# Performance work log

Hardware: AMD Instinct MI355X
Metric: run time of the kernel (lower is better)

## Reference

```python
import jax, jax.numpy as jnp
import numpy as np

B, S, IN, HID, H, D, FF = 8, 2048, 512, 512, 8, 64, 2048
EPS = 1e-5


def layer_norm(x, g, b):
    m = jnp.mean(x, axis=-1, keepdims=True)
    v = jnp.mean(jnp.square(x - m), axis=-1, keepdims=True)
    return (x - m) * jax.lax.rsqrt(v + EPS) * g + b


def delta_rule(q, k, v, beta):
    # q,k,v: [S,B,H,D]; beta: [S,B,H,1]
    # W_t = W_{t-1} + beta_t*(v_t - W_{t-1} k_t) k_t^T ; out_t = W_t q_t
    def step(W, inp):
        qt, kt, vt, bt = inp
        wk = jnp.einsum('bhde,bhe->bhd', W, kt)
        v_new = bt * (vt - wk)
        W = W + jnp.einsum('bhd,bhe->bhde', v_new, kt)
        out = jnp.einsum('bhde,bhe->bhd', W, qt)
        return W, out

    bsz = q.shape[1]
    W0 = jnp.zeros((bsz, H, D, D), dtype=q.dtype)
    _, outs = jax.lax.scan(step, W0, (q, k, v, beta))
    return outs  # [S,B,H,D]


def fast_ff(x, ln_g, ln_b, slow_w, out_w):
    # x: [S,B,HID]
    slen, bsz, _ = x.shape
    h = layer_norm(x, ln_g, ln_b)
    qkvb = jnp.einsum('sbi,oi->sbo', h, slow_w).reshape(slen, bsz, H, 3 * D + 1)
    q, k, v, beta = jnp.split(qkvb, [D, 2 * D, 3 * D], axis=-1)
    q = jax.nn.softmax(q, axis=-1)
    k = jax.nn.softmax(k, axis=-1)
    beta = jax.nn.sigmoid(beta)
    attn = delta_rule(q, k, v, beta)  # [S,B,H,D]
    o = jnp.einsum('sbd,od->sbo', attn.reshape(slen, bsz, H * D), out_w)
    return x + o


def ffn(x, ln_g, ln_b, w1, b1, w2, b2):
    h = layer_norm(x, ln_g, ln_b)
    h = jax.nn.relu(jnp.einsum('sbi,fi->sbf', h, w1) + b1)
    return x + jnp.einsum('sbf,of->sbo', h, w2) + b2


def setup_inputs() -> dict:
    key = jax.random.key(0)
    ks = jax.random.split(key, 8)
    s = 0.02
    return {
        'x': jax.random.normal(ks[0], (B, S, IN), jnp.float32),
        'ip_w': s * jax.random.normal(ks[1], (HID, IN), jnp.float32),
        'ip_b': jnp.zeros((HID,), jnp.float32),
        'fw_ln_g': jnp.ones((2, HID), jnp.float32),
        'fw_ln_b': jnp.zeros((2, HID), jnp.float32),
        'fw_slow_w': s * jax.random.normal(ks[2], (2, H * (3 * D + 1), HID), jnp.float32),
        'fw_out_w': s * jax.random.normal(ks[3], (2, HID, H * D), jnp.float32),
        'ff_ln_g': jnp.ones((HID,), jnp.float32),
        'ff_ln_b': jnp.zeros((HID,), jnp.float32),
        'ff_w1': s * jax.random.normal(ks[4], (FF, HID), jnp.float32),
        'ff_b1': jnp.zeros((FF,), jnp.float32),
        'ff_w2': s * jax.random.normal(ks[5], (HID, FF), jnp.float32),
        'ff_b2': jnp.zeros((HID,), jnp.float32),
    }


def reference(x, ip_w, ip_b, fw_ln_g, fw_ln_b, fw_slow_w, fw_out_w,
              ff_ln_g, ff_ln_b, ff_w1, ff_b1, ff_w2, ff_b2):
    out = jnp.einsum('bsi,hi->bsh', x, ip_w) + ip_b  # input_proj
    out = out.transpose(1, 0, 2)  # [S,B,HID]
    out = fast_ff(out, fw_ln_g[0], fw_ln_b[0], fw_slow_w[0], fw_out_w[0])
    out = ffn(out, ff_ln_g, ff_ln_b, ff_w1, ff_b1, ff_w2, ff_b2)
    out = fast_ff(out, fw_ln_g[1], fw_ln_b[1], fw_slow_w[1], fw_out_w[1])
    return out.transpose(1, 0, 2)  # [B,S,HID]
```

## Files before the change

### kernel.cpp

```cpp
#include <hip/hip_runtime.h>
#include <hip/hip_bf16.h>

#define B_    8
#define S_    2048
#define HID_  512
#define H_    8
#define D_    64
#define FF_   2048
#define QN_   1664
#define NCH_  32
#define SLOWSTRIDE (1544 * 512)

typedef unsigned short u16;
typedef __attribute__((ext_vector_type(8))) short short8;
typedef __attribute__((ext_vector_type(4))) float f32x4;

__device__ __forceinline__ u16 f2bf(float x) {
  unsigned u = __builtin_bit_cast(unsigned, x);
  unsigned r = (u + 0x7FFFu + ((u >> 16) & 1u)) >> 16;
  return (u16)r;
}
__device__ __forceinline__ float bf2f(u16 v) {
  return __builtin_bit_cast(float, (unsigned)v << 16);
}
__device__ __forceinline__ void gload16(const void* g, void* l) {
  __builtin_amdgcn_global_load_lds(
      (const __attribute__((address_space(1))) unsigned int*)g,
      (__attribute__((address_space(3))) unsigned int*)l, 16, 0, 0);
}

template<int FS, int GS>
__device__ __forceinline__ void prod64(const u16* __restrict__ F,
                                       const u16* __restrict__ G,
                                       int wrow0, int lane, f32x4 acc[4])
{
  short8 f0 = *(const short8*)&F[(wrow0 + (lane & 15)) * FS + ((lane >> 4) * 8)];
  short8 f1 = *(const short8*)&F[(wrow0 + (lane & 15)) * FS + 32 + ((lane >> 4) * 8)];
  #pragma unroll
  for (int c0 = 0; c0 < 4; ++c0) {
    short8 g0 = *(const short8*)&G[(c0 * 16 + (lane & 15)) * GS + ((lane >> 4) * 8)];
    short8 g1 = *(const short8*)&G[(c0 * 16 + (lane & 15)) * GS + 32 + ((lane >> 4) * 8)];
    acc[c0] = __builtin_amdgcn_mfma_f32_16x16x32_bf16(f0, g0, acc[c0], 0, 0, 0);
    acc[c0] = __builtin_amdgcn_mfma_f32_16x16x32_bf16(f1, g1, acc[c0], 0, 0, 0);
  }
}

template<bool BIAS, bool RELU, bool RES, bool OUTBF, bool TRANS, bool QKVB>
__global__ __launch_bounds__(256, 4) void gemm_bf(
    const u16* __restrict__ A, const u16* __restrict__ W,
    const float* __restrict__ bias, const float* __restrict__ res,
    void* __restrict__ Cout, int M, int N, int K)
{
  __shared__ __align__(16) u16 SH[16384];
  const int tid = threadIdx.x, lane = tid & 63, wv = tid >> 6;
  const int bm = blockIdx.y * 128, bn = blockIdx.x * 128;
  const int wr = wv >> 1, wc = wv & 1;
  const int row16 = lane & 15, kg = lane >> 4;
  const int srow = lane >> 2;
  const int ssoff = ((lane & 3) ^ (srow & 3)) * 16;

  f32x4 acc[4][4] = {};
  const int ktiles = K >> 5;

  auto STAGE = [&](int buf, int kt) {
    u16* As = &SH[buf * 8192];
    u16* Bs = &SH[buf * 8192 + 4096];
    #pragma unroll
    for (int i = 0; i < 2; ++i) {
      const int r = i * 64 + wv * 16;
      const char* ga = (const char*)(A + (size_t)(bm + r + srow) * K + (size_t)kt * 32) + ssoff;
      gload16(ga, &As[r * 32]);
      const char* gw = (const char*)(W + (size_t)(bn + r + srow) * K + (size_t)kt * 32) + ssoff;
      gload16(gw, &Bs[r * 32]);
    }
  };

  STAGE(0, 0);
  __syncthreads();
  int buf = 0;
  for (int kt = 0; kt < ktiles; ++kt) {
    if (kt + 1 < ktiles) STAGE(buf ^ 1, kt + 1);
    const u16* As = &SH[buf * 8192];
    const u16* Bs = &SH[buf * 8192 + 4096];
    short8 af[4], bf_[4];
    #pragma unroll
    for (int m = 0; m < 4; ++m) {
      const int lrow = wr * 64 + m * 16 + row16;
      af[m] = *(const short8*)&As[lrow * 32 + (kg ^ (lrow & 3)) * 8];
    }
    #pragma unroll
    for (int n = 0; n < 4; ++n) {
      const int lrow = wc * 64 + n * 16 + row16;
      bf_[n] = *(const short8*)&Bs[lrow * 32 + (kg ^ (lrow & 3)) * 8];
    }
    #pragma unroll
    for (int m = 0; m < 4; ++m)
      #pragma unroll
      for (int n = 0; n < 4; ++n)
        acc[m][n] = __builtin_amdgcn_mfma_f32_16x16x32_bf16(af[m], bf_[n], acc[m][n], 0, 0, 0);
    __syncthreads();
    buf ^= 1;
  }

  if (QKVB) {
    const int span0 = bn + wc * 64;
    #pragma unroll
    for (int m = 0; m < 4; ++m) {
      #pragma unroll
      for (int j = 0; j < 4; ++j) {
        if (span0 < 1024) {
          float v0 = acc[m][0][j], v1 = acc[m][1][j];
          float v2 = acc[m][2][j], v3 = acc[m][3][j];
          float mx = fmaxf(fmaxf(v0, v1), fmaxf(v2, v3));
          #pragma unroll
          for (int off = 1; off < 16; off <<= 1) mx = fmaxf(mx, __shfl_xor(mx, off));
          float e0 = __expf(v0 - mx), e1 = __expf(v1 - mx);
          float e2 = __expf(v2 - mx), e3 = __expf(v3 - mx);
          float s = (e0 + e1) + (e2 + e3);
          #pragma unroll
          for (int off = 1; off < 16; off <<= 1) s += __shfl_xor(s, off);
          float r = 1.f / s;
          acc[m][0][j] = e0 * r; acc[m][1][j] = e1 * r;
          acc[m][2][j] = e2 * r; acc[m][3][j] = e3 * r;
        } else if (span0 >= 1536) {
          #pragma unroll
          for (int n = 0; n < 4; ++n)
            acc[m][n][j] = 1.f / (1.f + __expf(-acc[m][n][j]));
        }
      }
    }
  }

  float* LD = (float*)SH;
  #pragma unroll
  for (int p = 0; p < 4; ++p) {
    if (p) __syncthreads();
    if (wr == (p >> 1)) {
      #pragma unroll
      for (int mm = 0; mm < 2; ++mm) {
        const int m = (p & 1) * 2 + mm;
        #pragma unroll
        for (int n = 0; n < 4; ++n)
          #pragma unroll
          for (int j = 0; j < 4; ++j)
            LD[(mm * 16 + kg * 4 + j) * 132 + wc * 64 + n * 16 + row16] = acc[m][n][j];
      }
    }
    __syncthreads();
    #pragma unroll
    for (int step = 0; step < 4; ++step) {
      int linear = step * 256 + tid;
      int row = linear >> 5, q = linear & 31;
      float4 v = *(const float4*)&LD[row * 132 + q * 4];
      const int grow = bm + p * 32 + row;
      const int gcol = bn + q * 4;
      if (BIAS) {
        float4 b4 = *(const float4*)&bias[gcol];
        v.x += b4.x; v.y += b4.y; v.z += b4.z; v.w += b4.w;
      }
      if (RES) {
        float4 r4 = *(const float4*)&res[(size_t)grow * N + gcol];
        v.x += r4.x; v.y += r4.y; v.z += r4.z; v.w += r4.w;
      }
      if (RELU) {
        v.x = fmaxf(v.x, 0.f); v.y = fmaxf(v.y, 0.f);
        v.z = fmaxf(v.z, 0.f); v.w = fmaxf(v.w, 0.f);
      }
      size_t gr = TRANS ? ((size_t)(grow & 7) * S_ + (grow >> 3)) : (size_t)grow;
      if (OUTBF) {
        uint2 pk;
        pk.x = (unsigned)f2bf(v.x) | ((unsigned)f2bf(v.y) << 16);
        pk.y = (unsigned)f2bf(v.z) | ((unsigned)f2bf(v.w) << 16);
        *(uint2*)&((u16*)Cout)[gr * N + gcol] = pk;
      } else {
        *(float4*)&((float*)Cout)[gr * N + gcol] = v;
      }
    }
  }
}

__global__ __launch_bounds__(256) void conv_w(const float* __restrict__ s,
                                              u16* __restrict__ d, int n, int npad)
{
  int i = blockIdx.x * 256 + threadIdx.x;
  if (i < npad) d[i] = (i < n) ? f2bf(s[i]) : (u16)0;
}

__global__ __launch_bounds__(256) void conv_slow(const float* __restrict__ s,
                                                 u16* __restrict__ d)
{
  int r = blockIdx.x;
  int src;
  if (r < 512)       src = (r >> 6) * 193 + (r & 63);
  else if (r < 1024) src = ((r - 512) >> 6) * 193 + 64 + (r & 63);
  else if (r < 1536) src = ((r - 1024) >> 6) * 193 + 128 + (r & 63);
  else if (r < 1544) src = (r - 1536) * 193 + 192;
  else               src = -1;
  for (int c = threadIdx.x; c < 512; c += 256)
    d[(size_t)r * 512 + c] = (src >= 0) ? f2bf(s[(size_t)src * 512 + c]) : (u16)0;
}

__global__ __launch_bounds__(64) void conv_x(const float* __restrict__ x,
                                             u16* __restrict__ xbf)
{
  size_t m = blockIdx.x;
  size_t s = m >> 3, b = m & 7;
  const float4* src = (const float4*)(x + (b * (size_t)S_ + s) * HID_);
  float4 v0 = src[threadIdx.x], v1 = src[64 + threadIdx.x];
  u16* dst = xbf + m * HID_;
  uint2 p0, p1;
  p0.x = (unsigned)f2bf(v0.x) | ((unsigned)f2bf(v0.y) << 16);
  p0.y = (unsigned)f2bf(v0.z) | ((unsigned)f2bf(v0.w) << 16);
  p1.x = (unsigned)f2bf(v1.x) | ((unsigned)f2bf(v1.y) << 16);
  p1.y = (unsigned)f2bf(v1.z) | ((unsigned)f2bf(v1.w) << 16);
  *(uint2*)&dst[threadIdx.x * 4] = p0;
  *(uint2*)&dst[256 + threadIdx.x * 4] = p1;
}

__global__ __launch_bounds__(64) void ln_bf(const float* __restrict__ x,
    const float* __restrict__ g, const float* __restrict__ bt,
    u16* __restrict__ o)
{
  size_t row = blockIdx.x;
  int lane = threadIdx.x;
  const float4* xr = (const float4*)(x + row * HID_);
  float4 v0 = xr[lane];
  float4 v1 = xr[64 + lane];
  float s  = v0.x + v0.y + v0.z + v0.w + v1.x + v1.y + v1.z + v1.w;
  float ss = v0.x*v0.x + v0.y*v0.y + v0.z*v0.z + v0.w*v0.w
           + v1.x*v1.x + v1.y*v1.y + v1.z*v1.z + v1.w*v1.w;
  #pragma unroll
  for (int off = 32; off; off >>= 1) {
    s  += __shfl_xor(s, off);
    ss += __shfl_xor(ss, off);
  }
  float mean = s * (1.f / HID_);
  float inv  = rsqrtf(ss * (1.f / HID_) - mean * mean + 1e-5f);
  const float4* gv = (const float4*)g;
  const float4* bv = (const float4*)bt;
  float4 g0 = gv[lane], g1 = gv[64 + lane];
  float4 b0 = bv[lane], b1 = bv[64 + lane];
  uint2 p0, p1;
  p0.x = (unsigned)f2bf((v0.x - mean) * inv * g0.x + b0.x)
       | ((unsigned)f2bf((v0.y - mean) * inv * g0.y + b0.y) << 16);
  p0.y = (unsigned)f2bf((v0.z - mean) * inv * g0.z + b0.z)
       | ((unsigned)f2bf((v0.w - mean) * inv * g0.w + b0.w) << 16);
  p1.x = (unsigned)f2bf((v1.x - mean) * inv * g1.x + b1.x)
       | ((unsigned)f2bf((v1.y - mean) * inv * g1.y + b1.y) << 16);
  p1.y = (unsigned)f2bf((v1.z - mean) * inv * g1.z + b1.z)
       | ((unsigned)f2bf((v1.w - mean) * inv * g1.w + b1.w) << 16);
  u16* ov = o + row * HID_;
  *(uint2*)&ov[lane * 4] = p0;
  *(uint2*)&ov[256 + lane * 4] = p1;
}

__global__ __launch_bounds__(256, 3) void delta_p1(const u16* __restrict__ qf,
                                                   u16* __restrict__ MTg,
                                                   u16* __restrict__ Ng,
                                                   u16* __restrict__ CKg,
                                                   u16* __restrict__ U0Tg)
{
  __shared__ __align__(16) u16 Kb[64 * 72];
  __shared__ __align__(16) u16 AmKT[64 * 72];
  __shared__ __align__(16) u16 stV[16 * 72];
  __shared__ __align__(16) u16 stK[16 * 72];
  __shared__ __align__(16) u16 CKTb[64 * 72];
  __shared__ __align__(16) u16 U0Tb[64 * 72];
  __shared__ float bet[64];

  const int id5 = blockIdx.x, bh = id5 >> 5;
  const int b = bh & 7, h = bh >> 3, t0 = (id5 & 31) * 64;
  const int tid = threadIdx.x, lane = tid & 63, wv = tid >> 6;
  const int wid = wv, wrow0 = wv * 16;
  const size_t mb = (size_t)id5 * 4096;

  #pragma unroll
  for (int p = 0; p < 2; ++p) {
    int linear = p * 256 + tid, row = linear >> 3, seg = linear & 7;
    uint4 k4 = *(const uint4*)&qf[((size_t)(t0 + row) * B_ + b) * QN_ + 512 + h * 64 + seg * 8];
    *(short8*)&Kb[row * 72 + seg * 8] = __builtin_bit_cast(short8, k4);
  }
  if (tid < 64) bet[tid] = bf2f(qf[((size_t)(t0 + tid) * B_ + b) * QN_ + 1536 + h]);
  __syncthreads();

  {
    f32x4 a[4] = {};
    prod64<72, 72>(Kb, Kb, wrow0, lane, a);
    #pragma unroll
    for (int c0 = 0; c0 < 4; ++c0)
      #pragma unroll
      for (int j = 0; j < 4; ++j) {
        int row = wrow0 + (lane >> 4) * 4 + j, col = c0 * 16 + (lane & 15);
        AmKT[row * 72 + col] = f2bf(bet[row] * a[c0][j]);
      }
  }

  float uv[16], uk[16];
  #pragma unroll
  for (int i = 0; i < 16; ++i) {
    const int row = wrow0 + i;
    const float bt_ = bet[row];
    uv[i] = bt_ * bf2f(qf[((size_t)(t0 + row) * B_ + b) * QN_ + 1024 + h * 64 + lane]);
    uk[i] = bt_ * bf2f(Kb[row * 72 + lane]);
  }
  __syncthreads();

  #pragma unroll 1
  for (int blk = 0; blk < 4; ++blk) {
    if (wid == blk) {
      const int r0 = blk * 16;
      #pragma unroll
      for (int jj = 0; jj < 15; ++jj) {
        #pragma unroll
        for (int t = jj + 1; t < 16; ++t) {
          float a = bf2f(AmKT[(r0 + t) * 72 + r0 + jj]);
          uv[t] = fmaf(-a, uv[jj], uv[t]);
          uk[t] = fmaf(-a, uk[jj], uk[t]);
        }
      }
      #pragma unroll
      for (int i = 0; i < 16; ++i) {
        stV[i * 72 + lane] = f2bf(uv[i]);
        stK[i * 72 + lane] = f2bf(uk[i]);
      }
    }
    __syncthreads();
    if (wid > blk) {
      const int r0 = blk * 16;
      #pragma unroll
      for (int jj = 0; jj < 16; ++jj) {
        float sv = bf2f(stV[jj * 72 + lane]);
        float sk = bf2f(stK[jj * 72 + lane]);
        #pragma unroll
        for (int i = 0; i < 16; ++i) {
          float a = bf2f(AmKT[(wrow0 + i) * 72 + r0 + jj]);
          uv[i] = fmaf(-a, sv, uv[i]);
          uk[i] = fmaf(-a, sk, uk[i]);
        }
      }
    }
    __syncthreads();
  }

  #pragma unroll
  for (int i = 0; i < 16; ++i) {
    const int row = wrow0 + i;
    u16 ck = f2bf(uk[i]), u0 = f2bf(uv[i]);
    CKg[mb + (size_t)row * 64 + lane] = ck;
    CKTb[lane * 72 + row] = ck;
    U0Tb[lane * 72 + row] = u0;
  }
  {
    const int prow = tid >> 2, pc0 = (tid & 3) * 16;
    #pragma unroll
    for (int i = 0; i < 16; ++i)
      AmKT[prow * 72 + pc0 + i] = Kb[(pc0 + i) * 72 + prow];
  }
  __syncthreads();

  {
    f32x4 am[4] = {}, an[4] = {};
    prod64<72, 72>(AmKT, CKTb, wrow0, lane, am);
    prod64<72, 72>(U0Tb, AmKT, wrow0, lane, an);
    #pragma unroll
    for (int c0 = 0; c0 < 4; ++c0)
      #pragma unroll
      for (int j = 0; j < 4; ++j) {
        int row = wrow0 + (lane >> 4) * 4 + j, col = c0 * 16 + (lane & 15);
        MTg[mb + (size_t)row * 64 + col] = f2bf(am[c0][j]);
        Ng[mb + (size_t)row * 64 + col]  = f2bf(an[c0][j]);
      }
    const int prow = tid >> 2, pc0 = (tid & 3) * 16;
    short8 a0 = *(const short8*)&U0Tb[prow * 72 + pc0];
    short8 a1 = *(const short8*)&U0Tb[prow * 72 + pc0 + 8];
    *(uint4*)&U0Tg[mb + prow * 64 + pc0]     = __builtin_bit_cast(uint4, a0);
    *(uint4*)&U0Tg[mb + prow * 64 + pc0 + 8] = __builtin_bit_cast(uint4, a1);
  }
}

__global__ __launch_bounds__(256, 1) void delta_p2(const u16* __restrict__ MTg,
                                                   const u16* __restrict__ Ng,
                                                   u16* __restrict__ Wsnap)
{
  __shared__ float Ws[64][65];
  __shared__ __align__(16) u16 Wbf[64 * 72];
  __shared__ __align__(16) u16 MTb[64 * 72];
  __shared__ __align__(16) u16 Nb[64 * 72];
  const int bh = blockIdx.x;
  const int tid = threadIdx.x, lane = tid & 63, wv = tid >> 6, wrow0 = wv * 16;
  const int prow = tid >> 2, pc0 = (tid & 3) * 16;

  for (int i = tid; i < 64 * 65; i += 256) (&Ws[0][0])[i] = 0.f;
  for (int i = tid; i < 64 * 72; i += 256) Wbf[i] = 0;
  __syncthreads();

  size_t base = (size_t)bh * NCH_ * 4096;
  uint4 rm0 = *(const uint4*)&MTg[base + prow * 64 + pc0];
  uint4 rm1 = *(const uint4*)&MTg[base + prow * 64 + pc0 + 8];
  uint4 rn0 = *(const uint4*)&Ng[base + prow * 64 + pc0];
  uint4 rn1 = *(const uint4*)&Ng[base + prow * 64 + pc0 + 8];

  for (int j = 0; j < NCH_; ++j) {
    *(short8*)&MTb[prow * 72 + pc0]     = __builtin_bit_cast(short8, rm0);
    *(short8*)&MTb[prow * 72 + pc0 + 8] = __builtin_bit_cast(short8, rm1);
    *(short8*)&Nb[prow * 72 + pc0]      = __builtin_bit_cast(short8, rn0);
    *(short8*)&Nb[prow * 72 + pc0 + 8]  = __builtin_bit_cast(short8, rn1);
    {
      size_t sb = base + (size_t)j * 4096;
      short8 w0 = *(const short8*)&Wbf[prow * 72 + pc0];
      short8 w1 = *(const short8*)&Wbf[prow * 72 + pc0 + 8];
      *(uint4*)&Wsnap[sb + prow * 64 + pc0]     = __builtin_bit_cast(uint4, w0);
      *(uint4*)&Wsnap[sb + prow * 64 + pc0 + 8] = __builtin_bit_cast(uint4, w1);
    }
    if (j + 1 < NCH_) {
      size_t nb2 = base + (size_t)(j + 1) * 4096;
      rm0 = *(const uint4*)&MTg[nb2 + prow * 64 + pc0];
      rm1 = *(const uint4*)&MTg[nb2 + prow * 64 + pc0 + 8];
      rn0 = *(const uint4*)&Ng[nb2 + prow * 64 + pc0];
      rn1 = *(const uint4*)&Ng[nb2 + prow * 64 + pc0 + 8];
    }
    __syncthreads();
    f32x4 a[4] = {};
    prod64<72, 72>(Wbf, MTb, wrow0, lane, a);
    #pragma unroll
    for (int c0 = 0; c0 < 4; ++c0)
      #pragma unroll
      for (int jj = 0; jj < 4; ++jj) {
        int row = wrow0 + (lane >> 4) * 4 + jj, col = c0 * 16 + (lane & 15);
        float w = Ws[row][col] + bf2f(Nb[row * 72 + col]) - a[c0][jj];
        Ws[row][col] = w;
        Wbf[row * 72 + col] = f2bf(w);
      }
    __syncthreads();
  }
}

__global__ __launch_bounds__(256, 2) void delta_p3(const u16* __restrict__ qf,
                                                   const u16* __restrict__ Wsnap,
                                                   const u16* __restrict__ CKg,
                                                   const u16* __restrict__ U0Tg,
                                                   u16* __restrict__ attnb)
{
  __shared__ __align__(16) u16 Qb[64 * 72];
  __shared__ __align__(16) u16 Kb[64 * 72];
  __shared__ __align__(16) u16 W0b[64 * 72];
  __shared__ __align__(16) u16 CKb[64 * 72];
  __shared__ __align__(16) u16 U0Tb[64 * 72];
  __shared__ __align__(16) u16 Gb[64 * 72];
  __shared__ __align__(16) u16 UTb[64 * 72];

  const int id5 = blockIdx.x, bh = id5 >> 5;
  const int b = bh & 7, h = bh >> 3, t0 = (id5 & 31) * 64;
  const int tid = threadIdx.x, lane = tid & 63, wv = tid >> 6, wrow0 = wv * 16;
  const int prow = tid >> 2, pc0 = (tid & 3) * 16;
  const size_t mb = (size_t)id5 * 4096;

  #pragma unroll
  for (int p = 0; p < 2; ++p) {
    int linear = p * 256 + tid, row = linear >> 3, seg = linear & 7;
    size_t gb = ((size_t)(t0 + row) * B_ + b) * QN_;
    uint4 q4 = *(const uint4*)&qf[gb + h * 64 + seg * 8];
    uint4 k4 = *(const uint4*)&qf[gb + 512 + h * 64 + seg * 8];
    uint4 w4 = *(const uint4*)&Wsnap[mb + (size_t)row * 64 + seg * 8];
    *(short8*)&Qb[row * 72 + seg * 8]  = __builtin_bit_cast(short8, q4);
    *(short8*)&Kb[row * 72 + seg * 8]  = __builtin_bit_cast(short8, k4);
    *(short8*)&W0b[row * 72 + seg * 8] = __builtin_bit_cast(short8, w4);
  }
  {
    uint4 c0v = *(const uint4*)&CKg[mb + prow * 64 + pc0];
    uint4 c1v = *(const uint4*)&CKg[mb + prow * 64 + pc0 + 8];
    uint4 u0v = *(const uint4*)&U0Tg[mb + prow * 64 + pc0];
    uint4 u1v = *(const uint4*)&U0Tg[mb + prow * 64 + pc0 + 8];
    *(short8*)&CKb[prow * 72 + pc0]      = __builtin_bit_cast(short8, c0v);
    *(short8*)&CKb[prow * 72 + pc0 + 8]  = __builtin_bit_cast(short8, c1v);
    *(short8*)&U0Tb[prow * 72 + pc0]     = __builtin_bit_cast(short8, u0v);
    *(short8*)&U0Tb[prow * 72 + pc0 + 8] = __builtin_bit_cast(short8, u1v);
  }
  __syncthreads();

  f32x4 ag[4] = {}, ac[4] = {}, ab[4] = {};
  prod64<72, 72>(Qb, Kb, wrow0, lane, ag);
  prod64<72, 72>(W0b, CKb, wrow0, lane, ac);
  prod64<72, 72>(Qb, W0b, wrow0, lane, ab);

  #pragma unroll
  for (int c0 = 0; c0 < 4; ++c0)
    #pragma unroll
    for (int j = 0; j < 4; ++j) {
      int row = wrow0 + (lane >> 4) * 4 + j, col = c0 * 16 + (lane & 15);
      Gb[row * 72 + col]  = f2bf(col <= row ? ag[c0][j] : 0.f);
      UTb[row * 72 + col] = f2bf(bf2f(U0Tb[row * 72 + col]) - ac[c0][j]);
    }
  __syncthreads();

  prod64<72, 72>(Gb, UTb, wrow0, lane, ab);

  #pragma unroll
  for (int c0 = 0; c0 < 4; ++c0)
    #pragma unroll
    for (int j = 0; j < 4; ++j) {
      int row = wrow0 + (lane >> 4) * 4 + j, col = c0 * 16 + (lane & 15);
      attnb[((size_t)(t0 + row) * B_ + b) * HID_ + h * 64 + col] = f2bf(ab[c0][j]);
    }
}

extern "C" void kernel_launch(void* const* d_in, const int* in_sizes, int n_in,
                              void* d_out, int out_size, void* d_ws, size_t ws_size,
                              hipStream_t stream)
{
  const float* x        = (const float*)d_in[0];
  const float* ip_w     = (const float*)d_in[1];
  const float* ip_b     = (const float*)d_in[2];
  const float* fw_ln_g  = (const float*)d_in[3];
  const float* fw_ln_b  = (const float*)d_in[4];
  const float* fw_slow_w = (const float*)d_in[5];
  const float* fw_out_w  = (const float*)d_in[6];
  const float* ff_ln_g  = (const float*)d_in[7];
  const float* ff_ln_b  = (const float*)d_in[8];
  const float* ff_w1    = (const float*)d_in[9];
  const float* ff_b1    = (const float*)d_in[10];
  const float* ff_w2    = (const float*)d_in[11];
  const float* ff_b2    = (const float*)d_in[12];
  float* out = (float*)d_out;

  const int M = B_ * S_;
  const size_t matN = (size_t)64 * NCH_ * 4096;

  const size_t nIp = 512 * 512, nOut = 512 * 512;
  const size_t nSlow = (size_t)QN_ * 512;
  const size_t nW1 = (size_t)FF_ * 512, nW2 = (size_t)512 * FF_;
  const size_t nXbf = (size_t)M * HID_;
  const size_t poolElems = nIp + 2 * nSlow + 2 * nOut + nW1 + nW2 + nXbf + matN;

  size_t need = (size_t)M * HID_ * 4
              + ((size_t)M * QN_ + 2 * matN + poolElems) * 2;
  if (ws_size < need) return;

  float* cur   = (float*)d_ws;
  u16*   qkvbf = (u16*)(cur + (size_t)M * HID_);
  u16*   attnSlot = qkvbf + (size_t)M * QN_;
  u16*   MTg   = attnSlot;
  u16*   Ng    = MTg + matN;
  u16*   attnb = attnSlot;
  u16*   CKg   = (u16*)out;
  u16*   U0Tg  = CKg + matN;
  u16*   tmpbf = (u16*)out;
  u16*   hiddenb = qkvbf;

  u16* pool = attnSlot + 2 * matN;
  u16* ipwb   = pool;               pool += nIp;
  u16* slowb0 = pool;               pool += nSlow;
  u16* slowb1 = pool;               pool += nSlow;
  u16* outwb0 = pool;               pool += nOut;
  u16* outwb1 = pool;               pool += nOut;
  u16* w1b    = pool;               pool += nW1;
  u16* w2b    = pool;               pool += nW2;
  u16* Wsnap  = pool;               pool += matN;
  u16* xbf    = pool;

  dim3 blk(256);

  conv_w<<<(nIp + 255) / 256, blk, 0, stream>>>(ip_w, ipwb, nIp, nIp);
  conv_slow<<<QN_, blk, 0, stream>>>(fw_slow_w, slowb0);
  conv_slow<<<QN_, blk, 0, stream>>>(fw_slow_w + (size_t)SLOWSTRIDE, slowb1);
  conv_w<<<(nOut + 255) / 256, blk, 0, stream>>>(fw_out_w, outwb0, nOut, nOut);
  conv_w<<<(nOut + 255) / 256, blk, 0, stream>>>(fw_out_w + (size_t)512 * 512, outwb1, nOut, nOut);
  conv_w<<<(nW1 + 255) / 256, blk, 0, stream>>>(ff_w1, w1b, nW1, nW1);
  conv_w<<<(nW2 + 255) / 256, blk, 0, stream>>>(ff_w2, w2b, nW2, nW2);
  conv_x<<<M, 64, 0, stream>>>(x, xbf);

  gemm_bf<true, false, false, false, false, false><<<dim3(4, 128), blk, 0, stream>>>(
      xbf, ipwb, ip_b, nullptr, cur, M, HID_, HID_);

  for (int layer = 0; layer < 2; ++layer) {
    u16* slowb = layer ? slowb1 : slowb0;
    u16* outwb = layer ? outwb1 : outwb0;

    ln_bf<<<M, 64, 0, stream>>>(cur, fw_ln_g + layer * HID_, fw_ln_b + layer * HID_, tmpbf);
    gemm_bf<false, false, false, true, false, true><<<dim3(13, 128), blk, 0, stream>>>(
        tmpbf, slowb, nullptr, nullptr, qkvbf, M, QN_, HID_);
    delta_p1<<<64 * NCH_, 256, 0, stream>>>(qkvbf, MTg, Ng, CKg, U0Tg);
    delta_p2<<<64, 256, 0, stream>>>(MTg, Ng, Wsnap);
    delta_p3<<<64 * NCH_, 256, 0, stream>>>(qkvbf, Wsnap, CKg, U0Tg, attnb);
    if (layer == 0) {
      gemm_bf<false, false, true, false, false, false><<<dim3(4, 128), blk, 0, stream>>>(
          attnb, outwb, nullptr, cur, cur, M, HID_, HID_);
      ln_bf<<<M, 64, 0, stream>>>(cur, ff_ln_g, ff_ln_b, tmpbf);
      gemm_bf<true, true, false, true, false, false><<<dim3(16, 128), blk, 0, stream>>>(
          tmpbf, w1b, ff_b1, nullptr, hiddenb, M, FF_, HID_);
      gemm_bf<true, false, true, false, false, false><<<dim3(4, 128), blk, 0, stream>>>(
          hiddenb, w2b, ff_b2, cur, cur, M, HID_, FF_);
    } else {
      gemm_bf<false, false, true, false, true, false><<<dim3(4, 128), blk, 0, stream>>>(
          attnb, outwb, nullptr, cur, out, M, HID_, HID_);
    }
  }
}
```

Baseline: 543.9 us.

## Remap GEMM workgroups across XCDs and tune delta_p1 solve and LDS use

```diff
diff --git a/kernel.cpp b/kernel.cpp
--- a/kernel.cpp
+++ b/kernel.cpp
@@ -49,11 +49,13 @@
 __global__ __launch_bounds__(256, 4) void gemm_bf(
     const u16* __restrict__ A, const u16* __restrict__ W,
     const float* __restrict__ bias, const float* __restrict__ res,
-    void* __restrict__ Cout, int M, int N, int K)
+    void* __restrict__ Cout, int M, int N, int K, int nx)
 {
   __shared__ __align__(16) u16 SH[16384];
   const int tid = threadIdx.x, lane = tid & 63, wv = tid >> 6;
-  const int bm = blockIdx.y * 128, bn = blockIdx.x * 128;
+  const int nwg = gridDim.x;
+  const int l = ((blockIdx.x & 7) * (nwg >> 3)) + (blockIdx.x >> 3);
+  const int bm = (l / nx) * 128, bn = (l % nx) * 128;
   const int wr = wv >> 1, wc = wv & 1;
   const int row16 = lane & 15, kg = lane >> 4;
   const int srow = lane >> 2;
@@ -254,7 +256,7 @@
   *(uint2*)&ov[256 + lane * 4] = p1;
 }
 
-__global__ __launch_bounds__(256, 3) void delta_p1(const u16* __restrict__ qf,
+__global__ __launch_bounds__(256, 4) void delta_p1(const u16* __restrict__ qf,
                                                    u16* __restrict__ MTg,
                                                    u16* __restrict__ Ng,
                                                    u16* __restrict__ CKg,
@@ -262,11 +264,11 @@
 {
   __shared__ __align__(16) u16 Kb[64 * 72];
   __shared__ __align__(16) u16 AmKT[64 * 72];
-  __shared__ __align__(16) u16 stV[16 * 72];
-  __shared__ __align__(16) u16 stK[16 * 72];
   __shared__ __align__(16) u16 CKTb[64 * 72];
   __shared__ __align__(16) u16 U0Tb[64 * 72];
   __shared__ float bet[64];
+  u16* stK = CKTb;
+  u16* stV = U0Tb;
 
   const int id5 = blockIdx.x, bh = id5 >> 5;
   const int b = bh & 7, h = bh >> 3, t0 = (id5 & 31) * 64;
@@ -309,13 +311,18 @@
   for (int blk = 0; blk < 4; ++blk) {
     if (wid == blk) {
       const int r0 = blk * 16;
+      float areg[16];
+      #pragma unroll
+      for (int t = 0; t < 16; ++t)
+        areg[t] = bf2f(AmKT[(r0 + t) * 72 + r0 + (lane & 15)]);
       #pragma unroll
       for (int jj = 0; jj < 15; ++jj) {
+        float uvj = uv[jj], ukj = uk[jj];
         #pragma unroll
         for (int t = jj + 1; t < 16; ++t) {
-          float a = bf2f(AmKT[(r0 + t) * 72 + r0 + jj]);
-          uv[t] = fmaf(-a, uv[jj], uv[t]);
-          uk[t] = fmaf(-a, uk[jj], uk[t]);
+          float a = __shfl(areg[t], jj, 16);
+          uv[t] = fmaf(-a, uvj, uv[t]);
+          uk[t] = fmaf(-a, ukj, uk[t]);
         }
       }
       #pragma unroll
@@ -327,13 +334,17 @@
     __syncthreads();
     if (wid > blk) {
       const int r0 = blk * 16;
+      float areg[16];
+      #pragma unroll
+      for (int i = 0; i < 16; ++i)
+        areg[i] = bf2f(AmKT[(wrow0 + i) * 72 + r0 + (lane & 15)]);
       #pragma unroll
       for (int jj = 0; jj < 16; ++jj) {
         float sv = bf2f(stV[jj * 72 + lane]);
         float sk = bf2f(stK[jj * 72 + lane]);
         #pragma unroll
         for (int i = 0; i < 16; ++i) {
-          float a = bf2f(AmKT[(wrow0 + i) * 72 + r0 + jj]);
+          float a = __shfl(areg[i], jj, 16);
           uv[i] = fmaf(-a, sv, uv[i]);
           uk[i] = fmaf(-a, sk, uk[i]);
         }
@@ -342,20 +353,19 @@
     __syncthreads();
   }
 
-  #pragma unroll
-  for (int i = 0; i < 16; ++i) {
-    const int row = wrow0 + i;
-    u16 ck = f2bf(uk[i]), u0 = f2bf(uv[i]);
-    CKg[mb + (size_t)row * 64 + lane] = ck;
-    CKTb[lane * 72 + row] = ck;
-    U0Tb[lane * 72 + row] = u0;
-  }
   {
-    const int prow = tid >> 2, pc0 = (tid & 3) * 16;
-    #pragma unroll
-    for (int i = 0; i < 16; ++i)
-      AmKT[prow * 72 + pc0 + i] = Kb[(pc0 + i) * 72 + prow];
-  }
+    union { u16 u[16]; short8 s[2]; } pk, pu;
+    #pragma unroll
+    for (int i = 0; i < 16; ++i) { pk.u[i] = f2bf(uk[i]); pu.u[i] = f2bf(uv[i]); }
+    *(short8*)&CKTb[lane * 72 + wrow0]     = pk.s[0];
+    *(short8*)&CKTb[lane * 72 + wrow0 + 8] = pk.s[1];
+    *(short8*)&U0Tb[lane * 72 + wrow0]     = pu.s[0];
+    *(short8*)&U0Tb[lane * 72 + wrow0 + 8] = pu.s[1];
+  }
+  const int prow = tid >> 2, pc0 = (tid & 3) * 16;
+  #pragma unroll
+  for (int i = 0; i < 16; ++i)
+    AmKT[prow * 72 + pc0 + i] = Kb[(pc0 + i) * 72 + prow];
   __syncthreads();
 
   {
@@ -370,7 +380,11 @@
         MTg[mb + (size_t)row * 64 + col] = f2bf(am[c0][j]);
         Ng[mb + (size_t)row * 64 + col]  = f2bf(an[c0][j]);
       }
-    const int prow = tid >> 2, pc0 = (tid & 3) * 16;
+    union { u16 u[16]; uint4 v[2]; } pc;
+    #pragma unroll
+    for (int i = 0; i < 16; ++i) pc.u[i] = CKTb[(pc0 + i) * 72 + prow];
+    *(uint4*)&CKg[mb + prow * 64 + pc0]     = pc.v[0];
+    *(uint4*)&CKg[mb + prow * 64 + pc0 + 8] = pc.v[1];
     short8 a0 = *(const short8*)&U0Tb[prow * 72 + pc0];
     short8 a1 = *(const short8*)&U0Tb[prow * 72 + pc0 + 8];
     *(uint4*)&U0Tg[mb + prow * 64 + pc0]     = __builtin_bit_cast(uint4, a0);
@@ -569,30 +583,30 @@
   conv_w<<<(nW2 + 255) / 256, blk, 0, stream>>>(ff_w2, w2b, nW2, nW2);
   conv_x<<<M, 64, 0, stream>>>(x, xbf);
 
-  gemm_bf<true, false, false, false, false, false><<<dim3(4, 128), blk, 0, stream>>>(
-      xbf, ipwb, ip_b, nullptr, cur, M, HID_, HID_);
+  gemm_bf<true, false, false, false, false, false><<<4 * 128, blk, 0, stream>>>(
+      xbf, ipwb, ip_b, nullptr, cur, M, HID_, HID_, 4);
 
   for (int layer = 0; layer < 2; ++layer) {
     u16* slowb = layer ? slowb1 : slowb0;
     u16* outwb = layer ? outwb1 : outwb0;
 
     ln_bf<<<M, 64, 0, stream>>>(cur, fw_ln_g + layer * HID_, fw_ln_b + layer * HID_, tmpbf);
-    gemm_bf<false, false, false, true, false, true><<<dim3(13, 128), blk, 0, stream>>>(
-        tmpbf, slowb, nullptr, nullptr, qkvbf, M, QN_, HID_);
+    gemm_bf<false, false, false, true, false, true><<<13 * 128, blk, 0, stream>>>(
+        tmpbf, slowb, nullptr, nullptr, qkvbf, M, QN_, HID_, 13);
     delta_p1<<<64 * NCH_, 256, 0, stream>>>(qkvbf, MTg, Ng, CKg, U0Tg);
     delta_p2<<<64, 256, 0, stream>>>(MTg, Ng, Wsnap);
     delta_p3<<<64 * NCH_, 256, 0, stream>>>(qkvbf, Wsnap, CKg, U0Tg, attnb);
     if (layer == 0) {
-      gemm_bf<false, false, true, false, false, false><<<dim3(4, 128), blk, 0, stream>>>(
-          attnb, outwb, nullptr, cur, cur, M, HID_, HID_);
+      gemm_bf<false, false, true, false, false, false><<<4 * 128, blk, 0, stream>>>(
+          attnb, outwb, nullptr, cur, cur, M, HID_, HID_, 4);
       ln_bf<<<M, 64, 0, stream>>>(cur, ff_ln_g, ff_ln_b, tmpbf);
-      gemm_bf<true, true, false, true, false, false><<<dim3(16, 128), blk, 0, stream>>>(
-          tmpbf, w1b, ff_b1, nullptr, hiddenb, M, FF_, HID_);
-      gemm_bf<true, false, true, false, false, false><<<dim3(4, 128), blk, 0, stream>>>(
-          hiddenb, w2b, ff_b2, cur, cur, M, HID_, FF_);
+      gemm_bf<true, true, false, true, false, false><<<16 * 128, blk, 0, stream>>>(
+          tmpbf, w1b, ff_b1, nullptr, hiddenb, M, FF_, HID_, 16);
+      gemm_bf<true, false, true, false, false, false><<<4 * 128, blk, 0, stream>>>(
+          hiddenb, w2b, ff_b2, cur, cur, M, HID_, FF_, 4);
     } else {
-      gemm_bf<false, false, true, false, true, false><<<dim3(4, 128), blk, 0, stream>>>(
-          attnb, outwb, nullptr, cur, out, M, HID_, HID_);
-    }
-  }
-}
+      gemm_bf<false, false, true, false, true, false><<<4 * 128, blk, 0, stream>>>(
+          attnb, outwb, nullptr, cur, out, M, HID_, HID_, 4);
+    }
+  }
+}
```

Measured after the change: 552.7 us. Within noise of the previous version (+1.6%).
